# Kernel optimization log

Hardware: AMD Instinct MI355X
Metric: run time of the kernel (lower is better)

Reference implementation:

```python
import jax, jax.numpy as jnp
import numpy as np

INPUT_DIM = 128
OUTPUT_DIM = 64
EMBED_DIM = 3
B, S = 16, 2048
EPS = 1e-6


def setup_inputs() -> dict:
    key = jax.random.key(0)
    ks = jax.random.split(key, 8)
    scale = 0.05
    return {
        "x": jax.random.normal(ks[0], (B, S, INPUT_DIM), dtype=jnp.float32),
        "threshold": jnp.asarray(0.1, dtype=jnp.float32),
        "w1": jax.random.normal(ks[1], (INPUT_DIM, 2 * EMBED_DIM), dtype=jnp.float32) * scale,
        "b1": jnp.zeros((2 * EMBED_DIM,), dtype=jnp.float32),
        "w2": jax.random.normal(ks[2], (2 * EMBED_DIM, EMBED_DIM), dtype=jnp.float32) * scale,
        "b2": jnp.zeros((EMBED_DIM,), dtype=jnp.float32),
        "w3": jax.random.normal(ks[3], (4, OUTPUT_DIM), dtype=jnp.float32) * scale,
        "b3": jnp.zeros((OUTPUT_DIM,), dtype=jnp.float32),
    }


def reference(x, threshold, w1, b1, w2, b2, w3, b3):
    # phase-space embedding: Linear -> ReLU -> Linear   [B,S,E]
    h = jnp.maximum(x @ w1 + b1, 0.0) @ w2 + b2
    Bsz, Slen, _ = h.shape

    # pairwise euclidean distances (torch.cdist) per batch element [B,S,S]
    sq = jnp.sum(h * h, axis=-1)                         # [B,S]
    d2 = sq[:, :, None] + sq[:, None, :] - 2.0 * jnp.einsum('bse,bte->bst', h, h)
    dist = jnp.sqrt(jnp.maximum(d2, 0.0))

    # per-sample threshold = sigmoid(theta) * max(dist)
    thr = jax.nn.sigmoid(threshold) * jnp.max(dist, axis=(1, 2), keepdims=True)
    R = (dist < thr).astype(h.dtype)                     # recurrence matrix [B,S,S]

    total = jnp.sum(R, axis=(1, 2))                      # [B]
    rr = total / (Slen * Slen)                           # recurrence rate

    # sum of super-diagonals with offsets 1..min(S,10)-1
    idx = jnp.arange(Slen)
    off = idx[None, :] - idx[:, None]
    dmask = ((off >= 1) & (off <= min(Slen, 10) - 1)).astype(h.dtype)  # [S,S]
    diag_structures = jnp.einsum('bst,st->b', R, dmask)
    det = diag_structures / (total + EPS)

    # vertical structures: per column (over rows, axis=1), count runs of length >= 2.
    # a run of length>=2 starts at row i iff R[i]=1, R[i-1]=0 (or i=0), R[i+1]=1.
    prev = jnp.pad(R[:, :-1, :], ((0, 0), (1, 0), (0, 0)))
    nxt = jnp.pad(R[:, 1:, :], ((0, 0), (0, 1), (0, 0)))
    vert_structures = jnp.sum(R * (1.0 - prev) * nxt, axis=(1, 2))
    lam = vert_structures / (total + EPS)

    # 'entropy' term as written in the original (R is 0/1 valued)
    entr = -jnp.sum(R * jnp.log(R + EPS), axis=(1, 2))

    metrics = jnp.stack([rr, det, lam, entr], axis=-1)   # [B,4]
    return jnp.maximum(metrics @ w3 + b3, 0.0)           # [B,output_dim]
```

## Files before the change

kernel.cpp:

```cpp
#include <hip/hip_runtime.h>
#include <math.h>

#define B_ 16
#define S_ 2048
#define IN_DIM 128
#define E2 6
#define E_ 3
#define OUT_DIM 64


__global__ __launch_bounds__(256) void embed_kernel(
    const float* __restrict__ x, const float* __restrict__ w1,
    const float* __restrict__ b1, const float* __restrict__ w2,
    const float* __restrict__ b2, float* __restrict__ hws)
{
    int wave = threadIdx.x >> 6;
    int lane = threadIdx.x & 63;
#pragma unroll
    for (int rr = 0; rr < 4; ++rr) {
        int row = blockIdx.x * 16 + wave * 4 + rr;
        const float2* x2 = (const float2*)(x + (size_t)row * IN_DIM);
        float2 xv = x2[lane];
        const float* w1a = w1 + (2 * lane) * E2;
        float a[E2];
#pragma unroll
        for (int q = 0; q < E2; ++q)
            a[q] = xv.x * w1a[q] + xv.y * w1a[E2 + q];
#pragma unroll
        for (int q = 0; q < E2; ++q) {
#pragma unroll
            for (int off = 32; off >= 1; off >>= 1)
                a[q] += __shfl_xor(a[q], off, 64);
        }
        if (lane == 0) {
            float r[E2];
#pragma unroll
            for (int q = 0; q < E2; ++q) r[q] = fmaxf(a[q] + b1[q], 0.f);
            float h[E_];
#pragma unroll
            for (int e = 0; e < E_; ++e) {
                float s = b2[e];
#pragma unroll
                for (int q = 0; q < E2; ++q) s += r[q] * w2[q * E_ + e];
                h[e] = s;
            }
            float sq = h[0] * h[0] + h[1] * h[1] + h[2] * h[2];
            ((float4*)hws)[row] = make_float4(h[0], h[1], h[2], sq);
        }
    }
}

__global__ __launch_bounds__(256) void max_kernel(
    const float4* __restrict__ h4, float* __restrict__ pmax)
{
    int bid = blockIdx.x;
    int b  = bid >> 5;
    int rb = bid & 31;
    int r0 = rb * 64;
    const float4* hb = h4 + (size_t)b * S_;
    __shared__ float4 sh[64];
    if (threadIdx.x < 64) {
        float4 rv = hb[r0 + threadIdx.x];
        sh[threadIdx.x] = make_float4(-2.f * rv.x, -2.f * rv.y, -2.f * rv.z, rv.w);
    }
    float4 hj[8];
#pragma unroll
    for (int c = 0; c < 8; ++c) hj[c] = hb[c * 256 + threadIdx.x];
    __syncthreads();
    float mc[8];
#pragma unroll
    for (int c = 0; c < 8; ++c) mc[c] = -1e30f;
    float4 rv = sh[63];
#pragma unroll 4
    for (int k = 62; k >= 0; --k) {
        float4 nx = sh[k];
#pragma unroll
        for (int c = 0; c < 8; ++c) {
            float t = fmaf(hj[c].x, rv.x,
                      fmaf(hj[c].y, rv.y,
                      fmaf(hj[c].z, rv.z, rv.w)));
            mc[c] = fmaxf(mc[c], t);
        }
        rv = nx;
    }
#pragma unroll
    for (int c = 0; c < 8; ++c) {
        float t = fmaf(hj[c].x, rv.x,
                  fmaf(hj[c].y, rv.y,
                  fmaf(hj[c].z, rv.z, rv.w)));
        mc[c] = fmaxf(mc[c], t);
    }
    float m = -1e30f;
#pragma unroll
    for (int c = 0; c < 8; ++c) m = fmaxf(m, mc[c] + hj[c].w);
    m = fmaxf(m, 0.f);
#pragma unroll
    for (int off = 32; off >= 1; off >>= 1)
        m = fmaxf(m, __shfl_xor(m, off, 64));
    __shared__ float wmax[4];
    int lane = threadIdx.x & 63, wave = threadIdx.x >> 6;
    if (lane == 0) wmax[wave] = m;
    __syncthreads();
    if (threadIdx.x == 0) {
        float mm = fmaxf(fmaxf(wmax[0], wmax[1]), fmaxf(wmax[2], wmax[3]));
        pmax[bid] = mm;
    }
}

__global__ __launch_bounds__(256) void stats_kernel(
    const float4* __restrict__ h4, const float* __restrict__ theta,
    const float* __restrict__ pmax, int4* __restrict__ pstat)
{
    int bid = blockIdx.x;
    int b  = bid >> 5;
    int rb = bid & 31;
    int r0 = rb * 64;
    const float4* hb = h4 + (size_t)b * S_;
    __shared__ float4 sh[66];
    if (threadIdx.x < 66) {
        int r = r0 - 1 + threadIdx.x;
        r = r < 0 ? 0 : (r >= S_ ? S_ - 1 : r);
        float4 rv = hb[r];
        sh[threadIdx.x] = make_float4(-2.f * rv.x, -2.f * rv.y, -2.f * rv.z, rv.w);
    }
    float4 hj[8];
#pragma unroll
    for (int c = 0; c < 8; ++c) hj[c] = hb[c * 256 + threadIdx.x];
    __syncthreads();

    int lane = threadIdx.x & 63;
    float pm = pmax[b * 32 + (lane & 31)];
#pragma unroll
    for (int off = 16; off >= 1; off >>= 1)
        pm = fmaxf(pm, __shfl_xor(pm, off, 64));
    float maxd2 = pm;

    float sig   = 1.f / (1.f + expf(-theta[0]));
    float thr2  = sig * sig * maxd2;
    float thrc[8];
#pragma unroll
    for (int c = 0; c < 8; ++c) thrc[c] = thr2 - hj[c].w;

    unsigned mlo[8], mhi[8];
#pragma unroll
    for (int c = 0; c < 8; ++c) { mlo[c] = 0u; mhi[c] = 0u; }

    float4 rv = sh[64];
#pragma unroll 4
    for (int k = 63; k >= 32; --k) {
        float4 nx = sh[k];
#pragma unroll
        for (int c = 0; c < 8; ++c) {
            float t = fmaf(hj[c].x, rv.x,
                      fmaf(hj[c].y, rv.y,
                      fmaf(hj[c].z, rv.z, rv.w)));
            mhi[c] = mhi[c] * 2u + ((t < thrc[c]) ? 1u : 0u);
        }
        rv = nx;
    }
#pragma unroll 4
    for (int k = 31; k >= 0; --k) {
        float4 nx = sh[k];
#pragma unroll
        for (int c = 0; c < 8; ++c) {
            float t = fmaf(hj[c].x, rv.x,
                      fmaf(hj[c].y, rv.y,
                      fmaf(hj[c].z, rv.z, rv.w)));
            mlo[c] = mlo[c] * 2u + ((t < thrc[c]) ? 1u : 0u);
        }
        rv = nx;
    }
    float4 pr = rv;
    float4 nxr = sh[65];

    int total = 0, diag = 0, vert = 0;
#pragma unroll
    for (int c = 0; c < 8; ++c) {
        int j = c * 256 + threadIdx.x;
        unsigned long long m = ((unsigned long long)mhi[c] << 32) | mlo[c];
        total += __popcll(m);
        float tp = fmaf(hj[c].x, pr.x, fmaf(hj[c].y, pr.y, fmaf(hj[c].z, pr.z, pr.w)));
        float tn = fmaf(hj[c].x, nxr.x, fmaf(hj[c].y, nxr.y, fmaf(hj[c].z, nxr.z, nxr.w)));
        unsigned long long prevbit = (r0 > 0) ? ((tp < thrc[c]) ? 1ull : 0ull) : 0ull;
        unsigned long long nextbit = (r0 + 64 < S_) ? ((tn < thrc[c]) ? 1ull : 0ull) : 0ull;
        unsigned long long notprev = ~((m << 1) | prevbit);
        vert += __popcll(m & notprev & ((m >> 1) | (nextbit << 63)));
        int lo = j - 9 - r0, hi = j - 1 - r0;
        if (hi >= 0 && lo <= 63) {
            int l = lo < 0 ? 0 : lo;
            int h = hi > 63 ? 63 : hi;
            unsigned long long bandm = ((1ull << (h - l + 1)) - 1ull) << l;
            diag += __popcll(m & bandm);
        }
    }

    int dv = (diag << 16) | vert;
#pragma unroll
    for (int off = 32; off >= 1; off >>= 1) {
        total += __shfl_xor(total, off, 64);
        dv    += __shfl_xor(dv,    off, 64);
    }
    __shared__ int wsum[4][2];
    int wave = threadIdx.x >> 6;
    if (lane == 0) { wsum[wave][0] = total; wsum[wave][1] = dv; }
    __syncthreads();
    if (threadIdx.x == 0) {
        int t = 0, d = 0, v = 0;
#pragma unroll
        for (int w = 0; w < 4; ++w) {
            t += wsum[w][0];
            d += wsum[w][1] >> 16;
            v += wsum[w][1] & 0xFFFF;
        }
        pstat[bid] = make_int4(t, d, v, 0);
    }
}

__global__ __launch_bounds__(256) void finalize_kernel(
    const int4* __restrict__ pstat,
    const float* __restrict__ w3, const float* __restrict__ b3,
    float* __restrict__ out)
{
    __shared__ float stot[16], sdia[16], sver[16];
    int tid = threadIdx.x;
    if (tid < 16) {
        int t = 0, d = 0, v = 0;
        for (int i = 0; i < 32; ++i) {
            int4 p = pstat[tid * 32 + i];
            t += p.x; d += p.y; v += p.z;
        }
        stot[tid] = (float)t; sdia[tid] = (float)d; sver[tid] = (float)v;
    }
    __syncthreads();
#pragma unroll
    for (int q = 0; q < 4; ++q) {
        int idx = q * 256 + tid;
        int b = idx >> 6, o = idx & 63;
        float total = stot[b], diag = sdia[b], vert = sver[b];
        float rr  = total / (float)(S_ * S_);
        float det = diag / (total + 1e-6f);
        float lam = vert / (total + 1e-6f);
        float entr = -total * logf(1.0f + 1e-6f);
        float r = b3[o] + rr  * w3[0 * OUT_DIM + o]
                        + det * w3[1 * OUT_DIM + o]
                        + lam * w3[2 * OUT_DIM + o]
                        + entr * w3[3 * OUT_DIM + o];
        out[idx] = fmaxf(r, 0.f);
    }
}

extern "C" void kernel_launch(void* const* d_in, const int* in_sizes, int n_in,
                              void* d_out, int out_size, void* d_ws, size_t ws_size,
                              hipStream_t stream) {
    const float* x     = (const float*)d_in[0];
    const float* theta = (const float*)d_in[1];
    const float* w1    = (const float*)d_in[2];
    const float* b1    = (const float*)d_in[3];
    const float* w2    = (const float*)d_in[4];
    const float* b2    = (const float*)d_in[5];
    const float* w3    = (const float*)d_in[6];
    const float* b3    = (const float*)d_in[7];
    float* out = (float*)d_out;
    float* hws = (float*)d_ws;
    float* pmax = (float*)((char*)d_ws + 524288);
    int4*  pstat = (int4*)((char*)d_ws + 526336);

    hipLaunchKernelGGL(embed_kernel, dim3(B_ * S_ / 16), dim3(256), 0, stream,
                       x, w1, b1, w2, b2, hws);
    hipLaunchKernelGGL(max_kernel, dim3(B_ * 32), dim3(256), 0, stream,
                       (const float4*)hws, pmax);
    hipLaunchKernelGGL(stats_kernel, dim3(B_ * 32), dim3(256), 0, stream,
                       (const float4*)hws, theta, pmax, pstat);
    hipLaunchKernelGGL(finalize_kernel, dim3(1), dim3(256), 0, stream,
                       pstat, w3, b3, out);
}
```

Baseline: 111.7 us.

## Restructure embed reduction per 16-lane group and fuse finalize into stats via last-block atomic

```diff
diff --git a/kernel.cpp b/kernel.cpp
--- a/kernel.cpp
+++ b/kernel.cpp
@@ -16,43 +16,58 @@
 {
     int wave = threadIdx.x >> 6;
     int lane = threadIdx.x & 63;
-#pragma unroll
-    for (int rr = 0; rr < 4; ++rr) {
-        int row = blockIdx.x * 16 + wave * 4 + rr;
-        const float2* x2 = (const float2*)(x + (size_t)row * IN_DIM);
-        float2 xv = x2[lane];
-        const float* w1a = w1 + (2 * lane) * E2;
-        float a[E2];
+    int rig  = lane >> 4;
+    int g    = lane & 15;
+    int row  = blockIdx.x * 16 + wave * 4 + rig;
+
+    const float4* x4 = (const float4*)(x + (size_t)row * IN_DIM) + g * 2;
+    float4 xa = x4[0];
+    float4 xb = x4[1];
+    float xk[8] = {xa.x, xa.y, xa.z, xa.w, xb.x, xb.y, xb.z, xb.w};
+
+    const float4* w14 = (const float4*)(w1 + g * 8 * E2);
+    float w[48];
+#pragma unroll
+    for (int t = 0; t < 12; ++t) ((float4*)w)[t] = w14[t];
+
+    float a[E2];
+#pragma unroll
+    for (int q = 0; q < E2; ++q) a[q] = 0.f;
+#pragma unroll
+    for (int kk = 0; kk < 8; ++kk) {
 #pragma unroll
         for (int q = 0; q < E2; ++q)
-            a[q] = xv.x * w1a[q] + xv.y * w1a[E2 + q];
-#pragma unroll
-        for (int q = 0; q < E2; ++q) {
-#pragma unroll
-            for (int off = 32; off >= 1; off >>= 1)
-                a[q] += __shfl_xor(a[q], off, 64);
-        }
-        if (lane == 0) {
-            float r[E2];
-#pragma unroll
-            for (int q = 0; q < E2; ++q) r[q] = fmaxf(a[q] + b1[q], 0.f);
-            float h[E_];
-#pragma unroll
-            for (int e = 0; e < E_; ++e) {
-                float s = b2[e];
-#pragma unroll
-                for (int q = 0; q < E2; ++q) s += r[q] * w2[q * E_ + e];
-                h[e] = s;
-            }
-            float sq = h[0] * h[0] + h[1] * h[1] + h[2] * h[2];
-            ((float4*)hws)[row] = make_float4(h[0], h[1], h[2], sq);
-        }
+            a[q] = fmaf(xk[kk], w[kk * E2 + q], a[q]);
+    }
+
+#pragma unroll
+    for (int q = 0; q < E2; ++q) {
+#pragma unroll
+        for (int off = 8; off >= 1; off >>= 1)
+            a[q] += __shfl_xor(a[q], off, 64);
+    }
+
+    if (g == 0) {
+        float r[E2];
+#pragma unroll
+        for (int q = 0; q < E2; ++q) r[q] = fmaxf(a[q] + b1[q], 0.f);
+        float h[E_];
+#pragma unroll
+        for (int e = 0; e < E_; ++e) {
+            float s = b2[e];
+#pragma unroll
+            for (int q = 0; q < E2; ++q) s += r[q] * w2[q * E_ + e];
+            h[e] = s;
+        }
+        float sq = h[0] * h[0] + h[1] * h[1] + h[2] * h[2];
+        ((float4*)hws)[row] = make_float4(h[0], h[1], h[2], sq);
     }
 }
 
 __global__ __launch_bounds__(256) void max_kernel(
-    const float4* __restrict__ h4, float* __restrict__ pmax)
+    const float4* __restrict__ h4, float* __restrict__ pmax, int* __restrict__ fincnt)
 {
+    if (blockIdx.x == 0 && threadIdx.x == 0) *fincnt = 0;
     int bid = blockIdx.x;
     int b  = bid >> 5;
     int rb = bid & 31;
@@ -109,7 +124,10 @@
 
 __global__ __launch_bounds__(256) void stats_kernel(
     const float4* __restrict__ h4, const float* __restrict__ theta,
-    const float* __restrict__ pmax, int4* __restrict__ pstat)
+    const float* __restrict__ pmax, int4* __restrict__ pstat,
+    int* __restrict__ fincnt,
+    const float* __restrict__ w3, const float* __restrict__ b3,
+    float* __restrict__ out)
 {
     int bid = blockIdx.x;
     int b  = bid >> 5;
@@ -201,6 +219,7 @@
         dv    += __shfl_xor(dv,    off, 64);
     }
     __shared__ int wsum[4][2];
+    __shared__ int slast;
     int wave = threadIdx.x >> 6;
     if (lane == 0) { wsum[wave][0] = total; wsum[wave][1] = dv; }
     __syncthreads();
@@ -213,14 +232,14 @@
             v += wsum[w][1] & 0xFFFF;
         }
         pstat[bid] = make_int4(t, d, v, 0);
-    }
-}
-
-__global__ __launch_bounds__(256) void finalize_kernel(
-    const int4* __restrict__ pstat,
-    const float* __restrict__ w3, const float* __restrict__ b3,
-    float* __restrict__ out)
-{
+        __threadfence();
+        int done = atomicAdd(fincnt, 1);
+        slast = (done == (int)gridDim.x - 1) ? 1 : 0;
+    }
+    __syncthreads();
+    if (slast == 0) return;
+
+    __threadfence();
     __shared__ float stot[16], sdia[16], sver[16];
     int tid = threadIdx.x;
     if (tid < 16) {
@@ -235,12 +254,12 @@
 #pragma unroll
     for (int q = 0; q < 4; ++q) {
         int idx = q * 256 + tid;
-        int b = idx >> 6, o = idx & 63;
-        float total = stot[b], diag = sdia[b], vert = sver[b];
-        float rr  = total / (float)(S_ * S_);
-        float det = diag / (total + 1e-6f);
-        float lam = vert / (total + 1e-6f);
-        float entr = -total * logf(1.0f + 1e-6f);
+        int bb = idx >> 6, o = idx & 63;
+        float tt = stot[bb], dd = sdia[bb], vv = sver[bb];
+        float rr  = tt / (float)(S_ * S_);
+        float det = dd / (tt + 1e-6f);
+        float lam = vv / (tt + 1e-6f);
+        float entr = -tt * logf(1.0f + 1e-6f);
         float r = b3[o] + rr  * w3[0 * OUT_DIM + o]
                         + det * w3[1 * OUT_DIM + o]
                         + lam * w3[2 * OUT_DIM + o]
@@ -264,13 +283,12 @@
     float* hws = (float*)d_ws;
     float* pmax = (float*)((char*)d_ws + 524288);
     int4*  pstat = (int4*)((char*)d_ws + 526336);
+    int*   fincnt = (int*)((char*)d_ws + 534528);
 
     hipLaunchKernelGGL(embed_kernel, dim3(B_ * S_ / 16), dim3(256), 0, stream,
                        x, w1, b1, w2, b2, hws);
     hipLaunchKernelGGL(max_kernel, dim3(B_ * 32), dim3(256), 0, stream,
-                       (const float4*)hws, pmax);
+                       (const float4*)hws, pmax, fincnt);
     hipLaunchKernelGGL(stats_kernel, dim3(B_ * 32), dim3(256), 0, stream,
-                       (const float4*)hws, theta, pmax, pstat);
-    hipLaunchKernelGGL(finalize_kernel, dim3(1), dim3(256), 0, stream,
-                       pstat, w3, b3, out);
-}
+                       (const float4*)hws, theta, pmax, pstat, fincnt, w3, b3, out);
+}
```

New measurement: 109.6 us. No clear change (-1.8%).
